# Performance work log

Measured on AMD Instinct MI355X. Metric: run time of the kernel, lower is better.

The kernel has to match this reference:

```python
import jax, jax.numpy as jnp
import numpy as np

C, I, O = 32, 1024, 1024
B, T = 64, 512


def setup_inputs() -> dict:
    key = jax.random.key(0)
    kx, kc, kw, kb = jax.random.split(key, 4)
    x = jax.random.normal(kx, (B, T, I), dtype=jnp.float32)
    cat_ids = jax.random.randint(kc, (B,), 0, C)
    W = 0.02 * jax.random.normal(kw, (C, I, O), dtype=jnp.float32)
    b = jnp.zeros((C, O), dtype=jnp.float32)
    return {"x": x, "cat_ids": cat_ids, "W": W, "b": b}


def reference(x, cat_ids, W, b):
    # Per-category affine: y[b] = x[b] @ W[cat_ids[b]] + b[cat_ids[b]]
    selected_W = W[cat_ids]            # [B, I, O] (gathered per batch element)
    selected_b = b[cat_ids]            # [B, O]
    if x.ndim == 2:
        return jnp.einsum('bi,bio->bo', x, selected_W) + selected_b
    return jnp.einsum('bti,bio->bto', x, selected_W) + selected_b[:, None, :]
```

## Files before the change

### kernel.cpp

```cpp
#include <hip/hip_runtime.h>
#include <stdint.h>

#define CATS  32
#define DI    1024
#define DO    1024
#define NB    64
#define ST    512

#define BM 128
#define BN 128
#define BK 32
#define NSTEP (DI / BK)

typedef float  f32x4  __attribute__((ext_vector_type(4)));
typedef short  bf16x8 __attribute__((ext_vector_type(8)));

__device__ __forceinline__ uint32_t cvt_pk_bf16(float lo, float hi) {
    uint32_t r;
    asm("v_cvt_pk_bf16_f32 %0, %1, %2" : "=v"(r) : "v"(lo), "v"(hi));
    return r;
}

__global__ __launch_bounds__(256) void fused_cat_gemm_kernel(
        const float* __restrict__ x, const int* __restrict__ cat_ids,
        const float* __restrict__ W, const float* __restrict__ bias,
        float* __restrict__ out) {
    __shared__ __align__(16) unsigned short As[2][BM * BK];
    __shared__ __align__(16) unsigned short Bs[2][BN * BK];

    const int fb = blockIdx.x;
    const int vv = (fb & 7) * 256 + (fb >> 3);
    const int b     = vv >> 5;
    const int mbase = ((vv >> 3) & 3) * BM;
    const int nbase = (vv & 7) * BN;
    const int cat   = cat_ids[b];

    const int tid  = threadIdx.x;
    const int lane = tid & 63;
    const int w    = tid >> 6;
    const int wr   = w >> 1;
    const int wc   = w & 1;
    const int l15  = lane & 15;
    const int kg   = lane >> 4;
    const int koff = (kg ^ ((l15 >> 1) & 3)) * 8;

    const int am   = tid >> 3;
    const int ak   = (tid & 7) * 4;
    const int ac   = (ak >> 3) ^ ((am >> 1) & 3);
    const int aoff = am * BK + ac * 8 + (ak & 4);
    const float* gA = x + (size_t)(b * ST + mbase + am) * DI + ak;

    const int nq  = tid & 31;
    const int k2b = tid >> 5;
    const float* gB = W + (size_t)cat * DI * DO + nbase + nq * 4;

    f32x4 acc[4][4];
    #pragma unroll
    for (int mi = 0; mi < 4; ++mi)
        #pragma unroll
        for (int ni = 0; ni < 4; ++ni)
            acc[mi][ni] = (f32x4){0.f, 0.f, 0.f, 0.f};

    f32x4 ra[4];
    f32x4 rb0[2], rb1[2];

    auto LOADS = [&](int step) {
        #pragma unroll
        for (int q = 0; q < 4; ++q)
            ra[q] = *(const f32x4*)(gA + (size_t)q * 32 * DI + step * BK);
        #pragma unroll
        for (int u = 0; u < 2; ++u) {
            const float* p = gB + (size_t)(step * BK + (k2b + 8 * u) * 2) * DO;
            rb0[u] = *(const f32x4*)p;
            rb1[u] = *(const f32x4*)(p + DO);
        }
    };

    auto WRITES = [&](int bufi) {
        #pragma unroll
        for (int q = 0; q < 4; ++q) {
            uint2 pk;
            pk.x = cvt_pk_bf16(ra[q][0], ra[q][1]);
            pk.y = cvt_pk_bf16(ra[q][2], ra[q][3]);
            *(uint2*)&As[bufi][aoff + q * 32 * BK] = pk;
        }
        #pragma unroll
        for (int u = 0; u < 2; ++u) {
            const int k2 = k2b + 8 * u;
            #pragma unroll
            for (int j = 0; j < 4; ++j) {
                const int n = nq * 4 + j;
                const int c = (k2 >> 2) ^ ((n >> 1) & 3);
                *(uint32_t*)&Bs[bufi][n * BK + c * 8 + (k2 & 3) * 2] =
                    cvt_pk_bf16(rb0[u][j], rb1[u][j]);
            }
        }
    };

    LOADS(0);
    WRITES(0);
    __syncthreads();

    int buf = 0;
    #pragma unroll 1
    for (int step = 0; step < NSTEP; ++step) {
        if (step + 1 < NSTEP)
            LOADS(step + 1);

        bf16x8 af[4], bfr[4];
        #pragma unroll
        for (int mi = 0; mi < 4; ++mi)
            af[mi] = *(const bf16x8*)&As[buf][(wr * 64 + mi * 16 + l15) * BK + koff];
        #pragma unroll
        for (int ni = 0; ni < 4; ++ni)
            bfr[ni] = *(const bf16x8*)&Bs[buf][(wc * 64 + ni * 16 + l15) * BK + koff];

        #pragma unroll
        for (int mi = 0; mi < 4; ++mi)
            #pragma unroll
            for (int ni = 0; ni < 4; ++ni)
                acc[mi][ni] = __builtin_amdgcn_mfma_f32_16x16x32_bf16(
                                  af[mi], bfr[ni], acc[mi][ni], 0, 0, 0);

        if (step + 1 < NSTEP)
            WRITES(buf ^ 1);

        __syncthreads();
        buf ^= 1;
    }

    float bsv[4];
    #pragma unroll
    for (int ni = 0; ni < 4; ++ni)
        bsv[ni] = bias[(size_t)cat * DO + nbase + wc * 64 + ni * 16 + l15];

    #pragma unroll
    for (int mi = 0; mi < 4; ++mi) {
        const int rowb = mbase + wr * 64 + mi * 16 + kg * 4;
        #pragma unroll
        for (int r = 0; r < 4; ++r) {
            float* orow = out + (size_t)(b * ST + rowb + r) * DO
                              + nbase + wc * 64 + l15;
            #pragma unroll
            for (int ni = 0; ni < 4; ++ni)
                orow[ni * 16] = acc[mi][ni][r] + bsv[ni];
        }
    }
}

extern "C" void kernel_launch(void* const* d_in, const int* in_sizes, int n_in,
                              void* d_out, int out_size, void* d_ws, size_t ws_size,
                              hipStream_t stream) {
    const float* x    = (const float*)d_in[0];
    const int*   cats = (const int*)d_in[1];
    const float* W    = (const float*)d_in[2];
    const float* bias = (const float*)d_in[3];
    float*       out  = (float*)d_out;

    (void)d_ws; (void)ws_size;

    fused_cat_gemm_kernel<<<NB * (ST / BM) * (DO / BN), 256, 0, stream>>>(
        x, cats, W, bias, out);
}
```

Before: 428.9 us.

## Deepen global prefetch to two register sets and use LDS-only barriers

Keeps two register staging sets so global loads for step s+2 are issued two MFMA steps ahead, unrolling the main loop by two. Replaces __syncthreads with an lgkmcnt(0) wait plus s_barrier so outstanding global loads need not drain at each barrier. Also remaps the W load thread layout so each wave covers contiguous N columns, and sets launch bounds to two blocks per CU. The aim is to hide global memory latency better, at the cost of extra VGPRs that could hurt occupancy or spill.

```diff
diff --git a/kernel.cpp b/kernel.cpp
--- a/kernel.cpp
+++ b/kernel.cpp
@@ -21,7 +21,12 @@
     return r;
 }
 
-__global__ __launch_bounds__(256) void fused_cat_gemm_kernel(
+struct Regs {
+    f32x4 ra[4];
+    f32x4 rb0[2], rb1[2];
+};
+
+__global__ __launch_bounds__(256, 2) void fused_cat_gemm_kernel(
         const float* __restrict__ x, const int* __restrict__ cat_ids,
         const float* __restrict__ W, const float* __restrict__ bias,
         float* __restrict__ out) {
@@ -50,9 +55,9 @@
     const int aoff = am * BK + ac * 8 + (ak & 4);
     const float* gA = x + (size_t)(b * ST + mbase + am) * DI + ak;
 
-    const int nq  = tid & 31;
-    const int k2b = tid >> 5;
-    const float* gB = W + (size_t)cat * DI * DO + nbase + nq * 4;
+    const int bq  = tid >> 3;
+    const int bk2 = lane & 7;
+    const float* gB = W + (size_t)cat * DI * DO + nbase + bq * 4;
 
     f32x4 acc[4][4];
     #pragma unroll
@@ -61,73 +66,80 @@
         for (int ni = 0; ni < 4; ++ni)
             acc[mi][ni] = (f32x4){0.f, 0.f, 0.f, 0.f};
 
-    f32x4 ra[4];
-    f32x4 rb0[2], rb1[2];
-
-    auto LOADS = [&](int step) {
+    auto LOADS = [&](Regs& R, int step) {
         #pragma unroll
         for (int q = 0; q < 4; ++q)
-            ra[q] = *(const f32x4*)(gA + (size_t)q * 32 * DI + step * BK);
+            R.ra[q] = *(const f32x4*)(gA + (size_t)q * 32 * DI + step * BK);
         #pragma unroll
         for (int u = 0; u < 2; ++u) {
-            const float* p = gB + (size_t)(step * BK + (k2b + 8 * u) * 2) * DO;
-            rb0[u] = *(const f32x4*)p;
-            rb1[u] = *(const f32x4*)(p + DO);
+            const float* p = gB + (size_t)(step * BK + (bk2 + 8 * u) * 2) * DO;
+            R.rb0[u] = *(const f32x4*)p;
+            R.rb1[u] = *(const f32x4*)(p + DO);
         }
     };
 
-    auto WRITES = [&](int bufi) {
+    auto WRITES = [&](int bufi, Regs& R) {
         #pragma unroll
         for (int q = 0; q < 4; ++q) {
             uint2 pk;
-            pk.x = cvt_pk_bf16(ra[q][0], ra[q][1]);
-            pk.y = cvt_pk_bf16(ra[q][2], ra[q][3]);
+            pk.x = cvt_pk_bf16(R.ra[q][0], R.ra[q][1]);
+            pk.y = cvt_pk_bf16(R.ra[q][2], R.ra[q][3]);
             *(uint2*)&As[bufi][aoff + q * 32 * BK] = pk;
         }
         #pragma unroll
         for (int u = 0; u < 2; ++u) {
-            const int k2 = k2b + 8 * u;
+            const int k2 = bk2 + 8 * u;
             #pragma unroll
             for (int j = 0; j < 4; ++j) {
-                const int n = nq * 4 + j;
-                const int c = (k2 >> 2) ^ ((n >> 1) & 3);
+                const int n = bq * 4 + j;
+                const int c = ((k2 >> 2) ^ (n >> 1)) & 3;
                 *(uint32_t*)&Bs[bufi][n * BK + c * 8 + (k2 & 3) * 2] =
-                    cvt_pk_bf16(rb0[u][j], rb1[u][j]);
+                    cvt_pk_bf16(R.rb0[u][j], R.rb1[u][j]);
             }
         }
     };
 
-    LOADS(0);
-    WRITES(0);
-    __syncthreads();
-
-    int buf = 0;
-    #pragma unroll 1
-    for (int step = 0; step < NSTEP; ++step) {
-        if (step + 1 < NSTEP)
-            LOADS(step + 1);
-
+    auto MFMA_STEP = [&](int bufc) {
         bf16x8 af[4], bfr[4];
         #pragma unroll
         for (int mi = 0; mi < 4; ++mi)
-            af[mi] = *(const bf16x8*)&As[buf][(wr * 64 + mi * 16 + l15) * BK + koff];
+            af[mi] = *(const bf16x8*)&As[bufc][(wr * 64 + mi * 16 + l15) * BK + koff];
         #pragma unroll
         for (int ni = 0; ni < 4; ++ni)
-            bfr[ni] = *(const bf16x8*)&Bs[buf][(wc * 64 + ni * 16 + l15) * BK + koff];
-
+            bfr[ni] = *(const bf16x8*)&Bs[bufc][(wc * 64 + ni * 16 + l15) * BK + koff];
         #pragma unroll
         for (int mi = 0; mi < 4; ++mi)
             #pragma unroll
             for (int ni = 0; ni < 4; ++ni)
                 acc[mi][ni] = __builtin_amdgcn_mfma_f32_16x16x32_bf16(
                                   af[mi], bfr[ni], acc[mi][ni], 0, 0, 0);
+    };
 
-        if (step + 1 < NSTEP)
-            WRITES(buf ^ 1);
+    #define LGKM_BARRIER()                                      \
+        do {                                                    \
+            asm volatile("s_waitcnt lgkmcnt(0)" ::: "memory");  \
+            __builtin_amdgcn_s_barrier();                       \
+        } while (0)
 
-        __syncthreads();
-        buf ^= 1;
+    Regs r0, r1;
+    LOADS(r0, 0);
+    WRITES(0, r0);
+    LOADS(r1, 1);
+    LGKM_BARRIER();
+
+    #pragma unroll 1
+    for (int s = 0; s < NSTEP; s += 2) {
+        if (s + 2 < NSTEP) LOADS(r0, s + 2);
+        MFMA_STEP(0);
+        WRITES(1, r1);
+        LGKM_BARRIER();
+
+        if (s + 3 < NSTEP) LOADS(r1, s + 3);
+        MFMA_STEP(1);
+        if (s + 2 < NSTEP) WRITES(0, r0);
+        LGKM_BARRIER();
     }
+    #undef LGKM_BARRIER
 
     float bsv[4];
     #pragma unroll
```

Result: no change. 428.0 us (-0.2%).
